# Optimization experiments

Measured on AMD Instinct MI355X. Metric: run time of the kernel, lower is better.

## Reference

```python
import jax, jax.numpy as jnp
import numpy as np

N_NODES = 100000
N_EDGES = 1600000
BN_EPS = 1e-5
NUM_LAYER = 20


def setup_inputs() -> dict:
    key = jax.random.key(0)
    ks = jax.random.split(key, 10)
    inp = {
        "M": jax.random.normal(ks[0], (N_NODES, 3), dtype=jnp.float32),
        "H": jax.random.normal(ks[1], (N_EDGES, 3), dtype=jnp.float32),
        "edge_index": jax.random.randint(ks[2], (2, N_EDGES), 0, N_NODES, dtype=jnp.int32),
        # mlp_e: Linear(9,4) -> BN(4) -> ReLU -> Linear(4,3)
        "we_w1": jax.random.normal(ks[3], (9, 4), dtype=jnp.float32) * 0.3,
        "we_b1": jnp.zeros((4,), jnp.float32),
        "we_g1": jnp.ones((4,), jnp.float32),
        "we_be1": jnp.zeros((4,), jnp.float32),
        "we_w2": jax.random.normal(ks[4], (4, 3), dtype=jnp.float32) * 0.3,
        "we_b2": jnp.zeros((3,), jnp.float32),
        # mlp_v: Linear(6,3) -> BN(3) -> ReLU -> Linear(3,3)
        "wv_w1": jax.random.normal(ks[5], (6, 3), dtype=jnp.float32) * 0.3,
        "wv_b1": jnp.zeros((3,), jnp.float32),
        "wv_g1": jnp.ones((3,), jnp.float32),
        "wv_be1": jnp.zeros((3,), jnp.float32),
        "wv_w2": jax.random.normal(ks[6], (3, 3), dtype=jnp.float32) * 0.3,
        "wv_b2": jnp.zeros((3,), jnp.float32),
        # head: Linear(3,3) -> BN(3) -> ReLU -> Linear(3,2) -> Softmax
        "out_w1": jax.random.normal(ks[7], (3, 3), dtype=jnp.float32) * 0.3,
        "out_b1": jnp.zeros((3,), jnp.float32),
        "out_g": jnp.ones((3,), jnp.float32),
        "out_be": jnp.zeros((3,), jnp.float32),
        "out_w2": jax.random.normal(ks[8], (3, 2), dtype=jnp.float32) * 0.3,
        "out_b2": jnp.zeros((2,), jnp.float32),
    }
    return inp


def _bn(x, g, b):
    # BatchNorm1d in training mode: batch stats, biased variance
    m = jnp.mean(x, axis=0)
    v = jnp.mean(jnp.square(x - m), axis=0)
    return (x - m) * jax.lax.rsqrt(v + BN_EPS) * g + b


def reference(M, H, edge_index, we_w1, we_b1, we_g1, we_be1, we_w2, we_b2,
              wv_w1, wv_b1, wv_g1, wv_be1, wv_w2, wv_b2,
              out_w1, out_b1, out_g, out_be, out_w2, out_b2):
    src = edge_index[0]  # _j (source, flow=source_to_target)
    dst = edge_index[1]  # _i (target), also the aggregation index
    n = M.shape[0]

    def layer(carry, _):
        M, H = carry
        Mi = M[dst]  # [E,3] gather of target node feats
        Mj = M[src]  # [E,3] gather of source node feats
        e_in = jnp.concatenate([Mi, Mj, H], axis=1)  # [E,9]
        Hn = jax.nn.relu(_bn(e_in @ we_w1 + we_b1, we_g1, we_be1)) @ we_w2 + we_b2  # [E,3]
        v_in = jnp.concatenate([Mi, Hn], axis=1)  # [E,6]
        Mmsg = jax.nn.relu(_bn(v_in @ wv_w1 + wv_b1, wv_g1, wv_be1)) @ wv_w2 + wv_b2  # [E,3]
        Mn = jax.ops.segment_sum(Mmsg, dst, num_segments=n)  # scatter-add to targets
        return (Mn, Hn), None

    (M, H), _ = jax.lax.scan(layer, (M, H), None, length=NUM_LAYER)
    logits = jax.nn.relu(_bn(H @ out_w1 + out_b1, out_g, out_be)) @ out_w2 + out_b2  # [E,2]
    return jax.nn.softmax(logits, axis=1)
```

## Files before the change

kernel.cpp:

```cpp
#include <hip/hip_runtime.h>
#include <hip/hip_fp16.h>
#include <math.h>

#define NNODES 100000
#define NEDGES 1600000
#define NGROUP (NEDGES / 4)
#define NLAYERS 20
#define NB 256
#define BLK 256
#define GRIDE 1024
#define STRIDE (GRIDE * BLK)
#define GRIDL ((NGROUP + BLK - 1) / BLK)
#define NBLKN ((NNODES + 255) / 256)
#define GRIDN4 ((NNODES * 4 + BLK - 1) / BLK)

struct __align__(8) H4 { __half h[4]; };

template<int N>
__device__ __forceinline__ void block_stats_atomic(const float* vals, double* base) {
  __shared__ float sm[8][4];
  int lane = threadIdx.x & 63, wid = threadIdx.x >> 6;
  __syncthreads();
  #pragma unroll
  for (int n = 0; n < N; ++n) {
    float d = vals[n];
    #pragma unroll
    for (int o = 32; o > 0; o >>= 1) d += __shfl_down(d, o, 64);
    if (lane == 0) sm[n][wid] = d;
  }
  __syncthreads();
  if (threadIdx.x < N) {
    double s = (double)sm[threadIdx.x][0] + (double)sm[threadIdx.x][1]
             + (double)sm[threadIdx.x][2] + (double)sm[threadIdx.x][3];
    atomicAdd(base + threadIdx.x, s);
  }
}

template<int NS>
__device__ __forceinline__ void bank_reduce(const double* __restrict__ acc, double* res) {
  __shared__ double part[4][8];
  int t = threadIdx.x;
  double v[NS];
  #pragma unroll
  for (int s = 0; s < NS; ++s) v[s] = acc[t * 8 + s];
  #pragma unroll
  for (int o = 32; o > 0; o >>= 1)
    #pragma unroll
    for (int s = 0; s < NS; ++s) v[s] += __shfl_down(v[s], o, 64);
  if ((t & 63) == 0) {
    int w = t >> 6;
    #pragma unroll
    for (int s = 0; s < NS; ++s) part[w][s] = v[s];
  }
  __syncthreads();
  #pragma unroll
  for (int s = 0; s < NS; ++s) res[s] = part[0][s] + part[1][s] + part[2][s] + part[3][s];
}

__device__ __forceinline__ void compute_x(const float4 mi, const float4 mj,
    float h0, float h1, float h2,
    const float* __restrict__ w, const float* __restrict__ b, float* x) {
  #pragma unroll
  for (int j = 0; j < 4; ++j) {
    float t = b[j];
    t += mi.x * w[0 * 4 + j]; t += mi.y * w[1 * 4 + j]; t += mi.z * w[2 * 4 + j];
    t += mj.x * w[3 * 4 + j]; t += mj.y * w[4 * 4 + j]; t += mj.z * w[5 * 4 + j];
    t += h0 * w[6 * 4 + j];  t += h1 * w[7 * 4 + j];  t += h2 * w[8 * 4 + j];
    x[j] = t;
  }
}

__global__ void __launch_bounds__(BLK) kz(const float* __restrict__ Min,
                                          float* __restrict__ M,
                                          int* __restrict__ hist,
                                          double* __restrict__ accs) {
  int tid = blockIdx.x * BLK + threadIdx.x;
  for (int v = tid; v < NNODES; v += STRIDE) {
    float4 m;
    m.x = Min[3 * v]; m.y = Min[3 * v + 1]; m.z = Min[3 * v + 2]; m.w = 0.f;
    *(float4*)(M + 4 * (size_t)v) = m;
    hist[v] = 0;
  }
  for (int i = tid; i < 3 * NB * 8; i += STRIDE) accs[i] = 0.0;
}

__global__ void __launch_bounds__(BLK) khr(const int* __restrict__ dst,
                                           int* __restrict__ hist,
                                           int* __restrict__ rankpos) {
  int g = blockIdx.x * BLK + threadIdx.x;
  if (g >= NGROUP) return;
  int4 d4 = ((const int4*)dst)[g];
  int4 r;
  r.x = atomicAdd(&hist[d4.x], 1);
  r.y = atomicAdd(&hist[d4.y], 1);
  r.z = atomicAdd(&hist[d4.z], 1);
  r.w = atomicAdd(&hist[d4.w], 1);
  ((int4*)rankpos)[g] = r;
}

__global__ void __launch_bounds__(256) ksA(const int* __restrict__ hist,
                                           int* __restrict__ bsum) {
  __shared__ int sm[256];
  int i = blockIdx.x * 256 + threadIdx.x;
  sm[threadIdx.x] = (i < NNODES) ? hist[i] : 0;
  __syncthreads();
  for (int o = 128; o > 0; o >>= 1) {
    if (threadIdx.x < o) sm[threadIdx.x] += sm[threadIdx.x + o];
    __syncthreads();
  }
  if (threadIdx.x == 0) bsum[blockIdx.x] = sm[0];
}

__global__ void __launch_bounds__(512) ksB(const int* __restrict__ bsum,
                                           int* __restrict__ bbase) {
  __shared__ int sm[512];
  int t = threadIdx.x;
  sm[t] = (t < NBLKN) ? bsum[t] : 0;
  __syncthreads();
  for (int o = 1; o < 512; o <<= 1) {
    int v = (t >= o) ? sm[t - o] : 0;
    __syncthreads();
    sm[t] += v;
    __syncthreads();
  }
  if (t < NBLKN) bbase[t] = (t == 0) ? 0 : sm[t - 1];
}

__global__ void __launch_bounds__(256) ksC(const int* __restrict__ hist,
                                           const int* __restrict__ bbase,
                                           int* __restrict__ off,
                                           int* __restrict__ dp) {
  __shared__ int sm[256];
  int t = threadIdx.x;
  int i = blockIdx.x * 256 + t;
  int v = (i < NNODES) ? hist[i] : 0;
  sm[t] = v;
  __syncthreads();
  for (int o = 1; o < 256; o <<= 1) {
    int u = (t >= o) ? sm[t - o] : 0;
    __syncthreads();
    sm[t] += u;
    __syncthreads();
  }
  if (i < NNODES) {
    int ex = bbase[blockIdx.x] + sm[t] - v;
    off[i] = ex;
    for (int e = ex; e < ex + v; ++e) dp[e] = i;
  }
  if (i == 0) off[NNODES] = NEDGES;
}

__global__ void __launch_bounds__(BLK) kpk(const int* __restrict__ dp,
                                           int2* __restrict__ dpp) {
  int g = blockIdx.x * BLK + threadIdx.x;
  if (g >= NGROUP) return;
  int4 d4 = ((const int4*)dp)[g];
  int2 o;
  o.x = d4.x;
  o.y = (d4.y - d4.x) | ((d4.z - d4.x) << 8) | ((d4.w - d4.x) << 16);
  dpp[g] = o;
}

__global__ void __launch_bounds__(BLK) kp1(const int* __restrict__ dst,
                                           const int* __restrict__ off,
                                           int* __restrict__ rankpos,
                                           int* __restrict__ eperm) {
  int g = blockIdx.x * BLK + threadIdx.x;
  if (g >= NGROUP) return;
  int4 d4 = ((const int4*)dst)[g];
  int4 r4 = ((int4*)rankpos)[g];
  int4 p4;
  p4.x = off[d4.x] + r4.x;
  p4.y = off[d4.y] + r4.y;
  p4.z = off[d4.z] + r4.z;
  p4.w = off[d4.w] + r4.w;
  int e = 4 * g;
  eperm[p4.x] = e; eperm[p4.y] = e + 1; eperm[p4.z] = e + 2; eperm[p4.w] = e + 3;
  ((int4*)rankpos)[g] = p4;
}

__global__ void __launch_bounds__(BLK) kp2(const int* __restrict__ src,
                                           const float* __restrict__ Hin,
                                           const int* __restrict__ eperm,
                                           int* __restrict__ sp,
                                           __half* __restrict__ Hp) {
  int g = blockIdx.x * BLK + threadIdx.x;
  if (g >= NGROUP) return;
  int4 e4 = ((const int4*)eperm)[g];
  int4 s4;
  s4.x = src[e4.x];
  s4.y = src[e4.y];
  s4.z = src[e4.z];
  s4.w = src[e4.w];
  __half hh[12];
  int ee[4] = {e4.x, e4.y, e4.z, e4.w};
  #pragma unroll
  for (int k = 0; k < 4; ++k) {
    size_t e3 = 3 * (size_t)ee[k];
    hh[3 * k]     = __float2half(Hin[e3]);
    hh[3 * k + 1] = __float2half(Hin[e3 + 1]);
    hh[3 * k + 2] = __float2half(Hin[e3 + 2]);
  }
  ((int4*)sp)[g] = s4;
  H4* Hv = (H4*)(Hp + 12 * (size_t)g);
  H4 a, b, c;
  #pragma unroll
  for (int i = 0; i < 4; ++i) { a.h[i] = hh[i]; b.h[i] = hh[4 + i]; c.h[i] = hh[8 + i]; }
  Hv[0] = a; Hv[1] = b; Hv[2] = c;
}

__global__ void __launch_bounds__(BLK) k1(
    const float* __restrict__ M, const __half* __restrict__ H,
    __half* __restrict__ xb,
    const int* __restrict__ sp, const int2* __restrict__ dpp,
    const float* __restrict__ W1, const float* __restrict__ b1,
    double* __restrict__ acc1, double* __restrict__ acc2) {
  int g = blockIdx.x * BLK + threadIdx.x;
  if (blockIdx.x == 0)
    for (int i = threadIdx.x; i < NB * 8; i += BLK) acc2[i] = 0.0;

  float sx[4] = {0, 0, 0, 0}, sq[4] = {0, 0, 0, 0};
  if (g < NGROUP) {
    int4 s4 = ((const int4*)sp)[g];
    int2 dppg = dpp[g];
    int d0 = dppg.x;
    int d1 = d0 + (dppg.y & 255);
    int d2 = d0 + ((dppg.y >> 8) & 255);
    int d3 = d0 + ((dppg.y >> 16) & 255);
    const H4* Hv = (const H4*)(H + 12 * (size_t)g);
    H4 a = Hv[0], b = Hv[1], c = Hv[2];
    float hf[12];
    #pragma unroll
    for (int i = 0; i < 4; ++i) {
      hf[i] = __half2float(a.h[i]); hf[4 + i] = __half2float(b.h[i]); hf[8 + i] = __half2float(c.h[i]);
    }
    float4 mi0 = *(const float4*)(M + 4 * (size_t)d0);
    float4 mj0 = *(const float4*)(M + 4 * (size_t)s4.x);
    float4 mi1 = *(const float4*)(M + 4 * (size_t)d1);
    float4 mj1 = *(const float4*)(M + 4 * (size_t)s4.y);
    float4 mi2 = *(const float4*)(M + 4 * (size_t)d2);
    float4 mj2 = *(const float4*)(M + 4 * (size_t)s4.z);
    float4 mi3 = *(const float4*)(M + 4 * (size_t)d3);
    float4 mj3 = *(const float4*)(M + 4 * (size_t)s4.w);
    float x[4][4];
    compute_x(mi0, mj0, hf[0], hf[1], hf[2],  W1, b1, x[0]);
    compute_x(mi1, mj1, hf[3], hf[4], hf[5],  W1, b1, x[1]);
    compute_x(mi2, mj2, hf[6], hf[7], hf[8],  W1, b1, x[2]);
    compute_x(mi3, mj3, hf[9], hf[10], hf[11], W1, b1, x[3]);
    H4* xv = (H4*)xb + 4 * (size_t)g;
    #pragma unroll
    for (int k = 0; k < 4; ++k) {
      H4 xo;
      #pragma unroll
      for (int j = 0; j < 4; ++j) {
        __half hx = __float2half(x[k][j]);
        xo.h[j] = hx;
        float xr = __half2float(hx);
        sx[j] += xr; sq[j] += xr * xr;
      }
      xv[k] = xo;
    }
  }
  float vals[8] = {sx[0], sx[1], sx[2], sx[3], sq[0], sq[1], sq[2], sq[3]};
  block_stats_atomic<8>(vals, acc1 + (size_t)(blockIdx.x & (NB - 1)) * 8);
}

__global__ void __launch_bounds__(BLK) k2(
    const float* __restrict__ M, __half* __restrict__ Hn,
    const __half* __restrict__ xb, const int2* __restrict__ dpp,
    const float* __restrict__ g1, const float* __restrict__ be1,
    const float* __restrict__ W2, const float* __restrict__ b2,
    const float* __restrict__ V1, const float* __restrict__ vb1,
    const double* __restrict__ acc1, double* __restrict__ acc2,
    int isFinal,
    const float* __restrict__ OW1, const float* __restrict__ ob1,
    double* __restrict__ accF) {
  double red[8];
  bank_reduce<8>(acc1, red);
  float s1[4], t1[4];
  {
    const double invE = 1.0 / (double)NEDGES;
    #pragma unroll
    for (int j = 0; j < 4; ++j) {
      double m = red[j] * invE;
      double var = red[4 + j] * invE - m * m;
      double sc = (double)g1[j] / sqrt(var + 1e-5);
      s1[j] = (float)sc;
      t1[j] = (float)((double)be1[j] - m * sc);
    }
  }
  float sz[3] = {0, 0, 0}, szz[3] = {0, 0, 0}, sf[3] = {0, 0, 0}, sff[3] = {0, 0, 0};
  int g = blockIdx.x * BLK + threadIdx.x;
  if (g < NGROUP) {
    int2 dppg = dpp[g];
    int dd[4];
    dd[0] = dppg.x;
    dd[1] = dd[0] + (dppg.y & 255);
    dd[2] = dd[0] + ((dppg.y >> 8) & 255);
    dd[3] = dd[0] + ((dppg.y >> 16) & 255);
    float4 mi[4];
    mi[0] = *(const float4*)(M + 4 * (size_t)dd[0]);
    mi[1] = *(const float4*)(M + 4 * (size_t)dd[1]);
    mi[2] = *(const float4*)(M + 4 * (size_t)dd[2]);
    mi[3] = *(const float4*)(M + 4 * (size_t)dd[3]);
    const H4* xv = (const H4*)xb + 4 * (size_t)g;
    __half hh[12];
    #pragma unroll
    for (int k = 0; k < 4; ++k) {
      H4 xh = xv[k];
      float y[4];
      #pragma unroll
      for (int j = 0; j < 4; ++j)
        y[j] = fmaxf(__half2float(xh.h[j]) * s1[j] + t1[j], 0.f);
      float hr[3];
      #pragma unroll
      for (int c = 0; c < 3; ++c) {
        float v = b2[c] + y[0] * W2[0 * 3 + c] + y[1] * W2[1 * 3 + c]
                        + y[2] * W2[2 * 3 + c] + y[3] * W2[3 * 3 + c];
        __half hv = __float2half(v);
        hh[3 * k + c] = hv;
        hr[c] = __half2float(hv);
      }
      #pragma unroll
      for (int c = 0; c < 3; ++c) {
        float z = vb1[c] + mi[k].x * V1[0 * 3 + c] + mi[k].y * V1[1 * 3 + c] + mi[k].z * V1[2 * 3 + c]
                         + hr[0] * V1[3 * 3 + c] + hr[1] * V1[4 * 3 + c] + hr[2] * V1[5 * 3 + c];
        sz[c] += z; szz[c] += z * z;
      }
      if (isFinal) {
        #pragma unroll
        for (int c = 0; c < 3; ++c) {
          float f = ob1[c] + hr[0] * OW1[0 * 3 + c] + hr[1] * OW1[1 * 3 + c] + hr[2] * OW1[2 * 3 + c];
          sf[c] += f; sff[c] += f * f;
        }
      }
    }
    H4* Hw = (H4*)(Hn + 12 * (size_t)g);
    H4 oA, oB, oC;
    #pragma unroll
    for (int i = 0; i < 4; ++i) { oA.h[i] = hh[i]; oB.h[i] = hh[4 + i]; oC.h[i] = hh[8 + i]; }
    Hw[0] = oA; Hw[1] = oB; Hw[2] = oC;
  }
  size_t bank = (size_t)(blockIdx.x & (NB - 1)) * 8;
  float v6[6] = {sz[0], sz[1], sz[2], szz[0], szz[1], szz[2]};
  block_stats_atomic<6>(v6, acc2 + bank);
  if (isFinal) {
    float v6b[6] = {sf[0], sf[1], sf[2], sff[0], sff[1], sff[2]};
    block_stats_atomic<6>(v6b, accF + bank);
  }
}

__global__ void __launch_bounds__(BLK) k3(
    float* __restrict__ M, const __half* __restrict__ Hn,
    const int* __restrict__ off,
    const float* __restrict__ V1, const float* __restrict__ vb1,
    const float* __restrict__ vg1, const float* __restrict__ vbe1,
    const float* __restrict__ V2, const float* __restrict__ vb2,
    const double* __restrict__ acc2, double* __restrict__ acc1) {
  double red[6];
  bank_reduce<6>(acc2, red);
  float s2[3], t2[3];
  {
    const double invE = 1.0 / (double)NEDGES;
    #pragma unroll
    for (int c = 0; c < 3; ++c) {
      double m = red[c] * invE;
      double var = red[3 + c] * invE - m * m;
      double sc = (double)vg1[c] / sqrt(var + 1e-5);
      s2[c] = (float)sc;
      t2[c] = (float)((double)vbe1[c] - m * sc);
    }
  }
  if (blockIdx.x == 0)
    for (int i = threadIdx.x; i < NB * 8; i += BLK) acc1[i] = 0.0;

  int idx = blockIdx.x * BLK + threadIdx.x;
  int v = idx >> 2, q = idx & 3;
  if (v >= NNODES) return;
  float4 mi = *(const float4*)(M + 4 * (size_t)v);
  int e0 = off[v], e1 = off[v + 1];
  float a0 = 0.f, a1 = 0.f, a2v = 0.f;
  for (int e = e0 + q; e < e1; e += 4) {
    size_t e3 = 3 * (size_t)e;
    float h0 = __half2float(Hn[e3]), h1 = __half2float(Hn[e3 + 1]), h2 = __half2float(Hn[e3 + 2]);
    float y[3];
    #pragma unroll
    for (int c = 0; c < 3; ++c) {
      float z = vb1[c] + mi.x * V1[0 * 3 + c] + mi.y * V1[1 * 3 + c] + mi.z * V1[2 * 3 + c]
                       + h0 * V1[3 * 3 + c] + h1 * V1[4 * 3 + c] + h2 * V1[5 * 3 + c];
      y[c] = fmaxf(z * s2[c] + t2[c], 0.f);
    }
    a0  += vb2[0] + y[0] * V2[0] + y[1] * V2[3] + y[2] * V2[6];
    a1  += vb2[1] + y[0] * V2[1] + y[1] * V2[4] + y[2] * V2[7];
    a2v += vb2[2] + y[0] * V2[2] + y[1] * V2[5] + y[2] * V2[8];
  }
  a0  += __shfl_down(a0, 2, 4);  a0  += __shfl_down(a0, 1, 4);
  a1  += __shfl_down(a1, 2, 4);  a1  += __shfl_down(a1, 1, 4);
  a2v += __shfl_down(a2v, 2, 4); a2v += __shfl_down(a2v, 1, 4);
  if (q == 0) {
    float4 o; o.x = a0; o.y = a1; o.z = a2v; o.w = 0.f;
    *(float4*)(M + 4 * (size_t)v) = o;
  }
}

__global__ void __launch_bounds__(BLK) f2(
    const __half* __restrict__ H, const int* __restrict__ pos,
    const float* __restrict__ OW1, const float* __restrict__ ob1,
    const float* __restrict__ og, const float* __restrict__ obe,
    const float* __restrict__ OW2, const float* __restrict__ ob2,
    const double* __restrict__ accF, float* __restrict__ out) {
  double red[6];
  bank_reduce<6>(accF, red);
  float sF[3], tF[3];
  {
    const double invE = 1.0 / (double)NEDGES;
    #pragma unroll
    for (int c = 0; c < 3; ++c) {
      double m = red[c] * invE;
      double var = red[3 + c] * invE - m * m;
      double sc = (double)og[c] / sqrt(var + 1e-5);
      sF[c] = (float)sc;
      tF[c] = (float)((double)obe[c] - m * sc);
    }
  }
  int g = blockIdx.x * BLK + threadIdx.x;
  if (g >= NGROUP) return;
  int4 p4 = ((const int4*)pos)[g];
  int p[4] = {p4.x, p4.y, p4.z, p4.w};
  float2 o[4];
  #pragma unroll
  for (int k = 0; k < 4; ++k) {
    size_t p3 = 3 * (size_t)p[k];
    float h0 = __half2float(H[p3]), h1 = __half2float(H[p3 + 1]), h2 = __half2float(H[p3 + 2]);
    float y[3];
    #pragma unroll
    for (int c = 0; c < 3; ++c) {
      float f = ob1[c] + h0 * OW1[0 * 3 + c] + h1 * OW1[1 * 3 + c] + h2 * OW1[2 * 3 + c];
      y[c] = fmaxf(f * sF[c] + tF[c], 0.f);
    }
    float l0 = ob2[0] + y[0] * OW2[0] + y[1] * OW2[2] + y[2] * OW2[4];
    float l1 = ob2[1] + y[0] * OW2[1] + y[1] * OW2[3] + y[2] * OW2[5];
    float mx = fmaxf(l0, l1);
    float e0 = __expf(l0 - mx), e1 = __expf(l1 - mx);
    float inv = 1.f / (e0 + e1);
    o[k].x = e0 * inv; o[k].y = e1 * inv;
  }
  float4 oA, oB;
  oA.x = o[0].x; oA.y = o[0].y; oA.z = o[1].x; oA.w = o[1].y;
  oB.x = o[2].x; oB.y = o[2].y; oB.z = o[3].x; oB.w = o[3].y;
  ((float4*)out)[2 * (size_t)g] = oA;
  ((float4*)out)[2 * (size_t)g + 1] = oB;
}

extern "C" void kernel_launch(void* const* d_in, const int* in_sizes, int n_in,
                              void* d_out, int out_size, void* d_ws, size_t ws_size,
                              hipStream_t stream) {
  const float* M_in   = (const float*)d_in[0];
  const float* H_in   = (const float*)d_in[1];
  const int*   ei     = (const int*)d_in[2];
  const float* we_w1  = (const float*)d_in[3];
  const float* we_b1  = (const float*)d_in[4];
  const float* we_g1  = (const float*)d_in[5];
  const float* we_be1 = (const float*)d_in[6];
  const float* we_w2  = (const float*)d_in[7];
  const float* we_b2  = (const float*)d_in[8];
  const float* wv_w1  = (const float*)d_in[9];
  const float* wv_b1  = (const float*)d_in[10];
  const float* wv_g1  = (const float*)d_in[11];
  const float* wv_be1 = (const float*)d_in[12];
  const float* wv_w2  = (const float*)d_in[13];
  const float* wv_b2  = (const float*)d_in[14];
  const float* out_w1 = (const float*)d_in[15];
  const float* out_b1 = (const float*)d_in[16];
  const float* out_g  = (const float*)d_in[17];
  const float* out_be = (const float*)d_in[18];
  const float* out_w2 = (const float*)d_in[19];
  const float* out_b2 = (const float*)d_in[20];
  const int* src = ei;
  const int* dst = ei + NEDGES;

  float* ws = (float*)d_ws;
  float* M    = ws;
  __half* Hp  = (__half*)(ws + 400000);
  __half* xb  = (__half*)(ws + 2800000);
  int* ib      = (int*)(ws + 6000000);
  int* sp      = ib;
  int* dp      = ib + 1600000;
  int* rankpos = ib + 3200000;
  int2* dpp    = (int2*)(ib + 4800000);
  int* hist    = ib + 5600000;
  int* off     = ib + 5700000;
  int* bsum    = ib + 5800001;
  int* bbase   = ib + 5800401;
  double* accs = (double*)(ws + 6000000 + 5800802);
  double* acc1 = accs;
  double* acc2 = accs + NB * 8;
  double* accF = accs + 2 * NB * 8;
  int* eperm   = dp;

  kz<<<GRIDE, BLK, 0, stream>>>(M_in, M, hist, accs);
  khr<<<GRIDL, BLK, 0, stream>>>(dst, hist, rankpos);
  ksA<<<NBLKN, 256, 0, stream>>>(hist, bsum);
  ksB<<<1, 512, 0, stream>>>(bsum, bbase);
  ksC<<<NBLKN, 256, 0, stream>>>(hist, bbase, off, dp);
  kpk<<<GRIDL, BLK, 0, stream>>>(dp, dpp);
  kp1<<<GRIDL, BLK, 0, stream>>>(dst, off, rankpos, eperm);
  kp2<<<GRIDL, BLK, 0, stream>>>(src, H_in, eperm, sp, Hp);

  for (int l = 0; l < NLAYERS; ++l) {
    k1<<<GRIDL, BLK, 0, stream>>>(M, Hp, xb, sp, dpp, we_w1, we_b1, acc1, acc2);
    k2<<<GRIDL, BLK, 0, stream>>>(M, Hp, xb, dpp, we_g1, we_be1,
                                  we_w2, we_b2, wv_w1, wv_b1, acc1, acc2,
                                  (l == NLAYERS - 1) ? 1 : 0, out_w1, out_b1, accF);
    if (l < NLAYERS - 1)
      k3<<<GRIDN4, BLK, 0, stream>>>(
          M, Hp, off, wv_w1, wv_b1, wv_g1, wv_be1, wv_w2, wv_b2, acc2, acc1);
  }
  f2<<<GRIDL, BLK, 0, stream>>>(Hp, rankpos, out_w1, out_b1, out_g, out_be,
                                out_w2, out_b2, accF, (float*)d_out);
}
```

Before: 1.151 ms.

## Fuse all GNN layers into one persistent cooperative kernel with grid syncs

Replaces the per-layer k1/k2/k3 launches and the final softmax kernel with a single cooperative persistent kernel. It loops over layers and uses grid.sync between phases instead of kernel boundaries, with a grid sized from occupancy and capped at 768 blocks. The goal is to remove about 60 kernel launch gaps. In exchange, the capped grid gives less parallelism for the gather-heavy phases, and the kernel relies on cooperative launch support, falling back to the old path when that launch fails or during graph capture on the first call.

```diff
diff --git a/kernel.cpp b/kernel.cpp
--- a/kernel.cpp
+++ b/kernel.cpp
@@ -1,6 +1,9 @@
 #include <hip/hip_runtime.h>
+#include <hip/hip_cooperative_groups.h>
 #include <hip/hip_fp16.h>
 #include <math.h>
+
+namespace cg = cooperative_groups;
 
 #define NNODES 100000
 #define NEDGES 1600000
@@ -13,6 +16,7 @@
 #define GRIDL ((NGROUP + BLK - 1) / BLK)
 #define NBLKN ((NNODES + 255) / 256)
 #define GRIDN4 ((NNODES * 4 + BLK - 1) / BLK)
+#define GRIDC_MAX 768
 
 struct __align__(8) H4 { __half h[4]; };
 
@@ -39,6 +43,7 @@
 template<int NS>
 __device__ __forceinline__ void bank_reduce(const double* __restrict__ acc, double* res) {
   __shared__ double part[4][8];
+  __syncthreads();
   int t = threadIdx.x;
   double v[NS];
   #pragma unroll
@@ -209,6 +214,262 @@
   Hv[0] = a; Hv[1] = b; Hv[2] = c;
 }
 
+__device__ __forceinline__ void phaseA_body(int g,
+    const float* __restrict__ M, const __half* __restrict__ Hp,
+    __half* __restrict__ xb, const int* __restrict__ sp,
+    const int2* __restrict__ dpp, const float* __restrict__ W1,
+    const float* __restrict__ b1, float* sx, float* sq) {
+  int4 s4 = ((const int4*)sp)[g];
+  int2 dg = dpp[g];
+  int d0 = dg.x;
+  int d1 = d0 + (dg.y & 255);
+  int d2 = d0 + ((dg.y >> 8) & 255);
+  int d3 = d0 + ((dg.y >> 16) & 255);
+  const H4* Hv = (const H4*)(Hp + 12 * (size_t)g);
+  H4 a = Hv[0], b = Hv[1], c = Hv[2];
+  float hf[12];
+  #pragma unroll
+  for (int i = 0; i < 4; ++i) {
+    hf[i] = __half2float(a.h[i]); hf[4 + i] = __half2float(b.h[i]); hf[8 + i] = __half2float(c.h[i]);
+  }
+  float4 mi0 = *(const float4*)(M + 4 * (size_t)d0);
+  float4 mj0 = *(const float4*)(M + 4 * (size_t)s4.x);
+  float4 mi1 = *(const float4*)(M + 4 * (size_t)d1);
+  float4 mj1 = *(const float4*)(M + 4 * (size_t)s4.y);
+  float4 mi2 = *(const float4*)(M + 4 * (size_t)d2);
+  float4 mj2 = *(const float4*)(M + 4 * (size_t)s4.z);
+  float4 mi3 = *(const float4*)(M + 4 * (size_t)d3);
+  float4 mj3 = *(const float4*)(M + 4 * (size_t)s4.w);
+  float x[4][4];
+  compute_x(mi0, mj0, hf[0], hf[1], hf[2],  W1, b1, x[0]);
+  compute_x(mi1, mj1, hf[3], hf[4], hf[5],  W1, b1, x[1]);
+  compute_x(mi2, mj2, hf[6], hf[7], hf[8],  W1, b1, x[2]);
+  compute_x(mi3, mj3, hf[9], hf[10], hf[11], W1, b1, x[3]);
+  H4* xv = (H4*)xb + 4 * (size_t)g;
+  #pragma unroll
+  for (int k = 0; k < 4; ++k) {
+    H4 xo;
+    #pragma unroll
+    for (int j = 0; j < 4; ++j) {
+      __half hx = __float2half(x[k][j]);
+      xo.h[j] = hx;
+      float v = __half2float(hx);
+      sx[j] += v; sq[j] += v * v;
+    }
+    xv[k] = xo;
+  }
+}
+
+__device__ __forceinline__ void phaseB_body(int g, int isFinal,
+    const float* __restrict__ M, __half* __restrict__ Hp,
+    const __half* __restrict__ xb, const int2* __restrict__ dpp,
+    const float* s1, const float* t1,
+    const float* __restrict__ W2, const float* __restrict__ b2,
+    const float* __restrict__ V1, const float* __restrict__ vb1,
+    const float* __restrict__ OW1, const float* __restrict__ ob1,
+    float* sz, float* szz, float* sf, float* sff) {
+  int2 dg = dpp[g];
+  int dd[4];
+  dd[0] = dg.x;
+  dd[1] = dd[0] + (dg.y & 255);
+  dd[2] = dd[0] + ((dg.y >> 8) & 255);
+  dd[3] = dd[0] + ((dg.y >> 16) & 255);
+  float4 mi[4];
+  mi[0] = *(const float4*)(M + 4 * (size_t)dd[0]);
+  mi[1] = *(const float4*)(M + 4 * (size_t)dd[1]);
+  mi[2] = *(const float4*)(M + 4 * (size_t)dd[2]);
+  mi[3] = *(const float4*)(M + 4 * (size_t)dd[3]);
+  const H4* xv = (const H4*)xb + 4 * (size_t)g;
+  __half hh[12];
+  #pragma unroll
+  for (int k = 0; k < 4; ++k) {
+    H4 xh = xv[k];
+    float y[4];
+    #pragma unroll
+    for (int j = 0; j < 4; ++j)
+      y[j] = fmaxf(__half2float(xh.h[j]) * s1[j] + t1[j], 0.f);
+    float hr[3];
+    #pragma unroll
+    for (int c = 0; c < 3; ++c) {
+      float v = b2[c] + y[0] * W2[0 * 3 + c] + y[1] * W2[1 * 3 + c]
+                      + y[2] * W2[2 * 3 + c] + y[3] * W2[3 * 3 + c];
+      __half hv = __float2half(v);
+      hh[3 * k + c] = hv;
+      hr[c] = __half2float(hv);
+    }
+    #pragma unroll
+    for (int c = 0; c < 3; ++c) {
+      float z = vb1[c] + mi[k].x * V1[0 * 3 + c] + mi[k].y * V1[1 * 3 + c] + mi[k].z * V1[2 * 3 + c]
+                       + hr[0] * V1[3 * 3 + c] + hr[1] * V1[4 * 3 + c] + hr[2] * V1[5 * 3 + c];
+      sz[c] += z; szz[c] += z * z;
+    }
+    if (isFinal) {
+      #pragma unroll
+      for (int c = 0; c < 3; ++c) {
+        float f = ob1[c] + hr[0] * OW1[0 * 3 + c] + hr[1] * OW1[1 * 3 + c] + hr[2] * OW1[2 * 3 + c];
+        sf[c] += f; sff[c] += f * f;
+      }
+    }
+  }
+  H4* Hw = (H4*)(Hp + 12 * (size_t)g);
+  H4 oA, oB, oC;
+  #pragma unroll
+  for (int i = 0; i < 4; ++i) { oA.h[i] = hh[i]; oB.h[i] = hh[4 + i]; oC.h[i] = hh[8 + i]; }
+  Hw[0] = oA; Hw[1] = oB; Hw[2] = oC;
+}
+
+__device__ __forceinline__ void phaseC_body(int idx,
+    float* __restrict__ M, const __half* __restrict__ Hp,
+    const int* __restrict__ off,
+    const float* s2, const float* t2,
+    const float* __restrict__ V1, const float* __restrict__ vb1,
+    const float* __restrict__ V2, const float* __restrict__ vb2) {
+  int v = idx >> 2, q = idx & 3;
+  float4 mi = *(const float4*)(M + 4 * (size_t)v);
+  int e0 = off[v], e1 = off[v + 1];
+  float a0 = 0.f, a1 = 0.f, a2v = 0.f;
+  for (int e = e0 + q; e < e1; e += 4) {
+    size_t e3 = 3 * (size_t)e;
+    float h0 = __half2float(Hp[e3]), h1 = __half2float(Hp[e3 + 1]), h2 = __half2float(Hp[e3 + 2]);
+    float y[3];
+    #pragma unroll
+    for (int c = 0; c < 3; ++c) {
+      float z = vb1[c] + mi.x * V1[0 * 3 + c] + mi.y * V1[1 * 3 + c] + mi.z * V1[2 * 3 + c]
+                       + h0 * V1[3 * 3 + c] + h1 * V1[4 * 3 + c] + h2 * V1[5 * 3 + c];
+      y[c] = fmaxf(z * s2[c] + t2[c], 0.f);
+    }
+    a0  += vb2[0] + y[0] * V2[0] + y[1] * V2[3] + y[2] * V2[6];
+    a1  += vb2[1] + y[0] * V2[1] + y[1] * V2[4] + y[2] * V2[7];
+    a2v += vb2[2] + y[0] * V2[2] + y[1] * V2[5] + y[2] * V2[8];
+  }
+  a0  += __shfl_down(a0, 2, 4);  a0  += __shfl_down(a0, 1, 4);
+  a1  += __shfl_down(a1, 2, 4);  a1  += __shfl_down(a1, 1, 4);
+  a2v += __shfl_down(a2v, 2, 4); a2v += __shfl_down(a2v, 1, 4);
+  if (q == 0) {
+    float4 o; o.x = a0; o.y = a1; o.z = a2v; o.w = 0.f;
+    *(float4*)(M + 4 * (size_t)v) = o;
+  }
+}
+
+__device__ __forceinline__ void phaseF_body(int g,
+    const __half* __restrict__ Hp, const int* __restrict__ pos,
+    const float* sF, const float* tF,
+    const float* __restrict__ OW1, const float* __restrict__ ob1,
+    const float* __restrict__ OW2, const float* __restrict__ ob2,
+    float* __restrict__ outp) {
+  int4 p4 = ((const int4*)pos)[g];
+  int p[4] = {p4.x, p4.y, p4.z, p4.w};
+  float2 o[4];
+  #pragma unroll
+  for (int k = 0; k < 4; ++k) {
+    size_t p3 = 3 * (size_t)p[k];
+    float h0 = __half2float(Hp[p3]), h1 = __half2float(Hp[p3 + 1]), h2 = __half2float(Hp[p3 + 2]);
+    float y[3];
+    #pragma unroll
+    for (int c = 0; c < 3; ++c) {
+      float f = ob1[c] + h0 * OW1[0 * 3 + c] + h1 * OW1[1 * 3 + c] + h2 * OW1[2 * 3 + c];
+      y[c] = fmaxf(f * sF[c] + tF[c], 0.f);
+    }
+    float l0 = ob2[0] + y[0] * OW2[0] + y[1] * OW2[2] + y[2] * OW2[4];
+    float l1 = ob2[1] + y[0] * OW2[1] + y[1] * OW2[3] + y[2] * OW2[5];
+    float mx = fmaxf(l0, l1);
+    float e0 = __expf(l0 - mx), e1 = __expf(l1 - mx);
+    float inv = 1.f / (e0 + e1);
+    o[k].x = e0 * inv; o[k].y = e1 * inv;
+  }
+  float4 oA, oB;
+  oA.x = o[0].x; oA.y = o[0].y; oA.z = o[1].x; oA.w = o[1].y;
+  oB.x = o[2].x; oB.y = o[2].y; oB.z = o[3].x; oB.w = o[3].y;
+  ((float4*)outp)[2 * (size_t)g] = oA;
+  ((float4*)outp)[2 * (size_t)g + 1] = oB;
+}
+
+__device__ __forceinline__ void bn_coeff(const double* red, int n,
+    const float* g, const float* be, float* s, float* t) {
+  const double invE = 1.0 / (double)NEDGES;
+  for (int c = 0; c < n; ++c) {
+    double m = red[c] * invE;
+    double var = red[n + c] * invE - m * m;
+    double sc = (double)g[c] / sqrt(var + 1e-5);
+    s[c] = (float)sc;
+    t[c] = (float)((double)be[c] - m * sc);
+  }
+}
+
+__global__ void __launch_bounds__(BLK, 3) kloop(
+    float* __restrict__ M, __half* __restrict__ Hp, __half* __restrict__ xb,
+    const int* __restrict__ sp, const int2* __restrict__ dpp,
+    const int* __restrict__ off, const int* __restrict__ pos,
+    const float* __restrict__ W1, const float* __restrict__ b1,
+    const float* __restrict__ g1, const float* __restrict__ be1,
+    const float* __restrict__ W2, const float* __restrict__ b2,
+    const float* __restrict__ V1, const float* __restrict__ vb1,
+    const float* __restrict__ vg1, const float* __restrict__ vbe1,
+    const float* __restrict__ V2, const float* __restrict__ vb2,
+    const float* __restrict__ OW1, const float* __restrict__ ob1,
+    const float* __restrict__ og, const float* __restrict__ obe,
+    const float* __restrict__ OW2, const float* __restrict__ ob2,
+    double* __restrict__ acc1, double* __restrict__ acc2,
+    double* __restrict__ accF, float* __restrict__ outp) {
+  cg::grid_group grid = cg::this_grid();
+  const int tid = blockIdx.x * BLK + threadIdx.x;
+  const int gsize = gridDim.x * BLK;
+  const size_t bank = (size_t)(blockIdx.x & (NB - 1)) * 8;
+
+  for (int l = 0; l < NLAYERS; ++l) {
+    const int isFinal = (l == NLAYERS - 1);
+
+    if (blockIdx.x == 0)
+      for (int i = threadIdx.x; i < NB * 8; i += BLK) acc2[i] = 0.0;
+    float sx[4] = {0, 0, 0, 0}, sq[4] = {0, 0, 0, 0};
+    for (int g = tid; g < NGROUP; g += gsize)
+      phaseA_body(g, M, Hp, xb, sp, dpp, W1, b1, sx, sq);
+    {
+      float va[8] = {sx[0], sx[1], sx[2], sx[3], sq[0], sq[1], sq[2], sq[3]};
+      block_stats_atomic<8>(va, acc1 + bank);
+    }
+    grid.sync();
+
+    double red[8];
+    bank_reduce<8>(acc1, red);
+    float s1[4], t1[4];
+    bn_coeff(red, 4, g1, be1, s1, t1);
+    float sz[3] = {0, 0, 0}, szz[3] = {0, 0, 0}, sf[3] = {0, 0, 0}, sff[3] = {0, 0, 0};
+    for (int g = tid; g < NGROUP; g += gsize)
+      phaseB_body(g, isFinal, M, Hp, xb, dpp, s1, t1, W2, b2, V1, vb1, OW1, ob1,
+                  sz, szz, sf, sff);
+    {
+      float v6[6] = {sz[0], sz[1], sz[2], szz[0], szz[1], szz[2]};
+      block_stats_atomic<6>(v6, acc2 + bank);
+    }
+    if (isFinal) {
+      float v6b[6] = {sf[0], sf[1], sf[2], sff[0], sff[1], sff[2]};
+      block_stats_atomic<6>(v6b, accF + bank);
+      break;
+    }
+    grid.sync();
+
+    double r2[6];
+    bank_reduce<6>(acc2, r2);
+    float s2[3], t2[3];
+    bn_coeff(r2, 3, vg1, vbe1, s2, t2);
+    if (blockIdx.x == 0)
+      for (int i = threadIdx.x; i < NB * 8; i += BLK) acc1[i] = 0.0;
+    for (int idx = tid; idx < NNODES * 4; idx += gsize)
+      phaseC_body(idx, M, Hp, off, s2, t2, V1, vb1, V2, vb2);
+    grid.sync();
+  }
+
+  grid.sync();
+
+  double rF[6];
+  bank_reduce<6>(accF, rF);
+  float sF[3], tF[3];
+  bn_coeff(rF, 3, og, obe, sF, tF);
+  for (int g = tid; g < NGROUP; g += gsize)
+    phaseF_body(g, Hp, pos, sF, tF, OW1, ob1, OW2, ob2, outp);
+}
+
 __global__ void __launch_bounds__(BLK) k1(
     const float* __restrict__ M, const __half* __restrict__ H,
     __half* __restrict__ xb,
@@ -218,49 +479,9 @@
   int g = blockIdx.x * BLK + threadIdx.x;
   if (blockIdx.x == 0)
     for (int i = threadIdx.x; i < NB * 8; i += BLK) acc2[i] = 0.0;
-
   float sx[4] = {0, 0, 0, 0}, sq[4] = {0, 0, 0, 0};
-  if (g < NGROUP) {
-    int4 s4 = ((const int4*)sp)[g];
-    int2 dppg = dpp[g];
-    int d0 = dppg.x;
-    int d1 = d0 + (dppg.y & 255);
-    int d2 = d0 + ((dppg.y >> 8) & 255);
-    int d3 = d0 + ((dppg.y >> 16) & 255);
-    const H4* Hv = (const H4*)(H + 12 * (size_t)g);
-    H4 a = Hv[0], b = Hv[1], c = Hv[2];
-    float hf[12];
-    #pragma unroll
-    for (int i = 0; i < 4; ++i) {
-      hf[i] = __half2float(a.h[i]); hf[4 + i] = __half2float(b.h[i]); hf[8 + i] = __half2float(c.h[i]);
-    }
-    float4 mi0 = *(const float4*)(M + 4 * (size_t)d0);
-    float4 mj0 = *(const float4*)(M + 4 * (size_t)s4.x);
-    float4 mi1 = *(const float4*)(M + 4 * (size_t)d1);
-    float4 mj1 = *(const float4*)(M + 4 * (size_t)s4.y);
-    float4 mi2 = *(const float4*)(M + 4 * (size_t)d2);
-    float4 mj2 = *(const float4*)(M + 4 * (size_t)s4.z);
-    float4 mi3 = *(const float4*)(M + 4 * (size_t)d3);
-    float4 mj3 = *(const float4*)(M + 4 * (size_t)s4.w);
-    float x[4][4];
-    compute_x(mi0, mj0, hf[0], hf[1], hf[2],  W1, b1, x[0]);
-    compute_x(mi1, mj1, hf[3], hf[4], hf[5],  W1, b1, x[1]);
-    compute_x(mi2, mj2, hf[6], hf[7], hf[8],  W1, b1, x[2]);
-    compute_x(mi3, mj3, hf[9], hf[10], hf[11], W1, b1, x[3]);
-    H4* xv = (H4*)xb + 4 * (size_t)g;
-    #pragma unroll
-    for (int k = 0; k < 4; ++k) {
-      H4 xo;
-      #pragma unroll
-      for (int j = 0; j < 4; ++j) {
-        __half hx = __float2half(x[k][j]);
-        xo.h[j] = hx;
-        float xr = __half2float(hx);
-        sx[j] += xr; sq[j] += xr * xr;
-      }
-      xv[k] = xo;
-    }
-  }
+  if (g < NGROUP)
+    phaseA_body(g, M, H, xb, sp, dpp, W1, b1, sx, sq);
   float vals[8] = {sx[0], sx[1], sx[2], sx[3], sq[0], sq[1], sq[2], sq[3]};
   block_stats_atomic<8>(vals, acc1 + (size_t)(blockIdx.x & (NB - 1)) * 8);
 }
@@ -278,69 +499,12 @@
   double red[8];
   bank_reduce<8>(acc1, red);
   float s1[4], t1[4];
-  {
-    const double invE = 1.0 / (double)NEDGES;
-    #pragma unroll
-    for (int j = 0; j < 4; ++j) {
-      double m = red[j] * invE;
-      double var = red[4 + j] * invE - m * m;
-      double sc = (double)g1[j] / sqrt(var + 1e-5);
-      s1[j] = (float)sc;
-      t1[j] = (float)((double)be1[j] - m * sc);
-    }
-  }
+  bn_coeff(red, 4, g1, be1, s1, t1);
   float sz[3] = {0, 0, 0}, szz[3] = {0, 0, 0}, sf[3] = {0, 0, 0}, sff[3] = {0, 0, 0};
   int g = blockIdx.x * BLK + threadIdx.x;
-  if (g < NGROUP) {
-    int2 dppg = dpp[g];
-    int dd[4];
-    dd[0] = dppg.x;
-    dd[1] = dd[0] + (dppg.y & 255);
-    dd[2] = dd[0] + ((dppg.y >> 8) & 255);
-    dd[3] = dd[0] + ((dppg.y >> 16) & 255);
-    float4 mi[4];
-    mi[0] = *(const float4*)(M + 4 * (size_t)dd[0]);
-    mi[1] = *(const float4*)(M + 4 * (size_t)dd[1]);
-    mi[2] = *(const float4*)(M + 4 * (size_t)dd[2]);
-    mi[3] = *(const float4*)(M + 4 * (size_t)dd[3]);
-    const H4* xv = (const H4*)xb + 4 * (size_t)g;
-    __half hh[12];
-    #pragma unroll
-    for (int k = 0; k < 4; ++k) {
-      H4 xh = xv[k];
-      float y[4];
-      #pragma unroll
-      for (int j = 0; j < 4; ++j)
-        y[j] = fmaxf(__half2float(xh.h[j]) * s1[j] + t1[j], 0.f);
-      float hr[3];
-      #pragma unroll
-      for (int c = 0; c < 3; ++c) {
-        float v = b2[c] + y[0] * W2[0 * 3 + c] + y[1] * W2[1 * 3 + c]
-                        + y[2] * W2[2 * 3 + c] + y[3] * W2[3 * 3 + c];
-        __half hv = __float2half(v);
-        hh[3 * k + c] = hv;
-        hr[c] = __half2float(hv);
-      }
-      #pragma unroll
-      for (int c = 0; c < 3; ++c) {
-        float z = vb1[c] + mi[k].x * V1[0 * 3 + c] + mi[k].y * V1[1 * 3 + c] + mi[k].z * V1[2 * 3 + c]
-                         + hr[0] * V1[3 * 3 + c] + hr[1] * V1[4 * 3 + c] + hr[2] * V1[5 * 3 + c];
-        sz[c] += z; szz[c] += z * z;
-      }
-      if (isFinal) {
-        #pragma unroll
-        for (int c = 0; c < 3; ++c) {
-          float f = ob1[c] + hr[0] * OW1[0 * 3 + c] + hr[1] * OW1[1 * 3 + c] + hr[2] * OW1[2 * 3 + c];
-          sf[c] += f; sff[c] += f * f;
-        }
-      }
-    }
-    H4* Hw = (H4*)(Hn + 12 * (size_t)g);
-    H4 oA, oB, oC;
-    #pragma unroll
-    for (int i = 0; i < 4; ++i) { oA.h[i] = hh[i]; oB.h[i] = hh[4 + i]; oC.h[i] = hh[8 + i]; }
-    Hw[0] = oA; Hw[1] = oB; Hw[2] = oC;
-  }
+  if (g < NGROUP)
+    phaseB_body(g, isFinal, M, Hn, xb, dpp, s1, t1, W2, b2, V1, vb1, OW1, ob1,
+                sz, szz, sf, sff);
   size_t bank = (size_t)(blockIdx.x & (NB - 1)) * 8;
   float v6[6] = {sz[0], sz[1], sz[2], szz[0], szz[1], szz[2]};
   block_stats_atomic<6>(v6, acc2 + bank);
@@ -360,47 +524,12 @@
   double red[6];
   bank_reduce<6>(acc2, red);
   float s2[3], t2[3];
-  {
-    const double invE = 1.0 / (double)NEDGES;
-    #pragma unroll
-    for (int c = 0; c < 3; ++c) {
-      double m = red[c] * invE;
-      double var = red[3 + c] * invE - m * m;
-      double sc = (double)vg1[c] / sqrt(var + 1e-5);
-      s2[c] = (float)sc;
-      t2[c] = (float)((double)vbe1[c] - m * sc);
-    }
-  }
+  bn_coeff(red, 3, vg1, vbe1, s2, t2);
   if (blockIdx.x == 0)
     for (int i = threadIdx.x; i < NB * 8; i += BLK) acc1[i] = 0.0;
-
   int idx = blockIdx.x * BLK + threadIdx.x;
-  int v = idx >> 2, q = idx & 3;
-  if (v >= NNODES) return;
-  float4 mi = *(const float4*)(M + 4 * (size_t)v);
-  int e0 = off[v], e1 = off[v + 1];
-  float a0 = 0.f, a1 = 0.f, a2v = 0.f;
-  for (int e = e0 + q; e < e1; e += 4) {
-    size_t e3 = 3 * (size_t)e;
-    float h0 = __half2float(Hn[e3]), h1 = __half2float(Hn[e3 + 1]), h2 = __half2float(Hn[e3 + 2]);
-    float y[3];
-    #pragma unroll
-    for (int c = 0; c < 3; ++c) {
-      float z = vb1[c] + mi.x * V1[0 * 3 + c] + mi.y * V1[1 * 3 + c] + mi.z * V1[2 * 3 + c]
-                       + h0 * V1[3 * 3 + c] + h1 * V1[4 * 3 + c] + h2 * V1[5 * 3 + c];
-      y[c] = fmaxf(z * s2[c] + t2[c], 0.f);
-    }
-    a0  += vb2[0] + y[0] * V2[0] + y[1] * V2[3] + y[2] * V2[6];
-    a1  += vb2[1] + y[0] * V2[1] + y[1] * V2[4] + y[2] * V2[7];
-    a2v += vb2[2] + y[0] * V2[2] + y[1] * V2[5] + y[2] * V2[8];
-  }
-  a0  += __shfl_down(a0, 2, 4);  a0  += __shfl_down(a0, 1, 4);
-  a1  += __shfl_down(a1, 2, 4);  a1  += __shfl_down(a1, 1, 4);
-  a2v += __shfl_down(a2v, 2, 4); a2v += __shfl_down(a2v, 1, 4);
-  if (q == 0) {
-    float4 o; o.x = a0; o.y = a1; o.z = a2v; o.w = 0.f;
-    *(float4*)(M + 4 * (size_t)v) = o;
-  }
+  if ((idx >> 2) >= NNODES) return;
+  phaseC_body(idx, M, Hn, off, s2, t2, V1, vb1, V2, vb2);
 }
 
 __global__ void __launch_bounds__(BLK) f2(
@@ -412,44 +541,10 @@
   double red[6];
   bank_reduce<6>(accF, red);
   float sF[3], tF[3];
-  {
-    const double invE = 1.0 / (double)NEDGES;
-    #pragma unroll
-    for (int c = 0; c < 3; ++c) {
-      double m = red[c] * invE;
-      double var = red[3 + c] * invE - m * m;
-      double sc = (double)og[c] / sqrt(var + 1e-5);
-      sF[c] = (float)sc;
-      tF[c] = (float)((double)obe[c] - m * sc);
-    }
-  }
+  bn_coeff(red, 3, og, obe, sF, tF);
   int g = blockIdx.x * BLK + threadIdx.x;
   if (g >= NGROUP) return;
-  int4 p4 = ((const int4*)pos)[g];
-  int p[4] = {p4.x, p4.y, p4.z, p4.w};
-  float2 o[4];
-  #pragma unroll
-  for (int k = 0; k < 4; ++k) {
-    size_t p3 = 3 * (size_t)p[k];
-    float h0 = __half2float(H[p3]), h1 = __half2float(H[p3 + 1]), h2 = __half2float(H[p3 + 2]);
-    float y[3];
-    #pragma unroll
-    for (int c = 0; c < 3; ++c) {
-      float f = ob1[c] + h0 * OW1[0 * 3 + c] + h1 * OW1[1 * 3 + c] + h2 * OW1[2 * 3 + c];
-      y[c] = fmaxf(f * sF[c] + tF[c], 0.f);
-    }
-    float l0 = ob2[0] + y[0] * OW2[0] + y[1] * OW2[2] + y[2] * OW2[4];
-    float l1 = ob2[1] + y[0] * OW2[1] + y[1] * OW2[3] + y[2] * OW2[5];
-    float mx = fmaxf(l0, l1);
-    float e0 = __expf(l0 - mx), e1 = __expf(l1 - mx);
-    float inv = 1.f / (e0 + e1);
-    o[k].x = e0 * inv; o[k].y = e1 * inv;
-  }
-  float4 oA, oB;
-  oA.x = o[0].x; oA.y = o[0].y; oA.z = o[1].x; oA.w = o[1].y;
-  oB.x = o[2].x; oB.y = o[2].y; oB.z = o[3].x; oB.w = o[3].y;
-  ((float4*)out)[2 * (size_t)g] = oA;
-  ((float4*)out)[2 * (size_t)g + 1] = oB;
+  phaseF_body(g, H, pos, sF, tF, OW1, ob1, OW2, ob2, out);
 }
 
 extern "C" void kernel_launch(void* const* d_in, const int* in_sizes, int n_in,
@@ -480,9 +575,9 @@
   const int* dst = ei + NEDGES;
 
   float* ws = (float*)d_ws;
-  float* M    = ws;
-  __half* Hp  = (__half*)(ws + 400000);
-  __half* xb  = (__half*)(ws + 2800000);
+  float* M     = ws;
+  __half* Hp   = (__half*)(ws + 400000);
+  __half* xb   = (__half*)(ws + 2800000);
   int* ib      = (int*)(ws + 6000000);
   int* sp      = ib;
   int* dp      = ib + 1600000;
@@ -497,6 +592,7 @@
   double* acc2 = accs + NB * 8;
   double* accF = accs + 2 * NB * 8;
   int* eperm   = dp;
+  float* outp  = (float*)d_out;
 
   kz<<<GRIDE, BLK, 0, stream>>>(M_in, M, hist, accs);
   khr<<<GRIDL, BLK, 0, stream>>>(dst, hist, rankpos);
@@ -507,15 +603,58 @@
   kp1<<<GRIDL, BLK, 0, stream>>>(dst, off, rankpos, eperm);
   kp2<<<GRIDL, BLK, 0, stream>>>(src, H_in, eperm, sp, Hp);
 
-  for (int l = 0; l < NLAYERS; ++l) {
-    k1<<<GRIDL, BLK, 0, stream>>>(M, Hp, xb, sp, dpp, we_w1, we_b1, acc1, acc2);
-    k2<<<GRIDL, BLK, 0, stream>>>(M, Hp, xb, dpp, we_g1, we_be1,
-                                  we_w2, we_b2, wv_w1, wv_b1, acc1, acc2,
-                                  (l == NLAYERS - 1) ? 1 : 0, out_w1, out_b1, accF);
-    if (l < NLAYERS - 1)
-      k3<<<GRIDN4, BLK, 0, stream>>>(
-          M, Hp, off, wv_w1, wv_b1, wv_g1, wv_be1, wv_w2, wv_b2, acc2, acc1);
-  }
-  f2<<<GRIDL, BLK, 0, stream>>>(Hp, rankpos, out_w1, out_b1, out_g, out_be,
-                                out_w2, out_b2, accF, (float*)d_out);
-}
+  static int g_coop = -1;
+  static int g_grid = 0;
+  if (g_grid == 0) {
+    int dev = 0;
+    (void)hipGetDevice(&dev);
+    int nCU = 0;
+    if (hipDeviceGetAttribute(&nCU, hipDeviceAttributeMultiprocessorCount, dev)
+          != hipSuccess || nCU <= 0) nCU = 256;
+    int perCU = 0;
+    if (hipOccupancyMaxActiveBlocksPerMultiprocessor(&perCU, kloop, BLK, 0)
+          != hipSuccess || perCU <= 0) perCU = 1;
+    long cap = (long)perCU * nCU;
+    g_grid = (int)(cap < GRIDC_MAX ? cap : GRIDC_MAX);
+    if (g_grid < 64) g_grid = 64;
+  }
+
+  hipStreamCaptureStatus cst = hipStreamCaptureStatusNone;
+  (void)hipStreamIsCapturing(stream, &cst);
+  const bool capturing = (cst != hipStreamCaptureStatusNone);
+  bool try_coop = (g_coop == 1) || (g_coop == -1 && !capturing);
+
+  bool coop_done = false;
+  if (try_coop) {
+    void* kargs[] = {
+      (void*)&M, (void*)&Hp, (void*)&xb, (void*)&sp, (void*)&dpp, (void*)&off, (void*)&rankpos,
+      (void*)&we_w1, (void*)&we_b1, (void*)&we_g1, (void*)&we_be1, (void*)&we_w2, (void*)&we_b2,
+      (void*)&wv_w1, (void*)&wv_b1, (void*)&wv_g1, (void*)&wv_be1, (void*)&wv_w2, (void*)&wv_b2,
+      (void*)&out_w1, (void*)&out_b1, (void*)&out_g, (void*)&out_be, (void*)&out_w2, (void*)&out_b2,
+      (void*)&acc1, (void*)&acc2, (void*)&accF, (void*)&outp
+    };
+    hipError_t e = hipLaunchCooperativeKernel((void*)kloop, dim3(g_grid), dim3(BLK),
+                                              kargs, 0, stream);
+    if (e == hipSuccess) {
+      coop_done = true;
+      if (g_coop == -1) g_coop = 1;
+    } else {
+      g_coop = 0;
+      (void)hipGetLastError();
+    }
+  }
+
+  if (!coop_done) {
+    for (int l = 0; l < NLAYERS; ++l) {
+      k1<<<GRIDL, BLK, 0, stream>>>(M, Hp, xb, sp, dpp, we_w1, we_b1, acc1, acc2);
+      k2<<<GRIDL, BLK, 0, stream>>>(M, Hp, xb, dpp, we_g1, we_be1,
+                                    we_w2, we_b2, wv_w1, wv_b1, acc1, acc2,
+                                    (l == NLAYERS - 1) ? 1 : 0, out_w1, out_b1, accF);
+      if (l < NLAYERS - 1)
+        k3<<<GRIDN4, BLK, 0, stream>>>(
+            M, Hp, off, wv_w1, wv_b1, wv_g1, wv_be1, wv_w2, wv_b2, acc2, acc1);
+    }
+    f2<<<GRIDL, BLK, 0, stream>>>(Hp, rankpos, out_w1, out_b1, out_g, out_be,
+                                  out_w2, out_b2, accF, outp);
+  }
+}
```

Measured after the change: 2.765 ms. 2.4x slower.
